# Kernel tuning notes

Hardware: AMD Instinct MI355X
Metric: run time of the kernel (lower is better)

The kernel has to match this reference:

```python
import jax, jax.numpy as jnp
import numpy as np

N_HEADS = 4
ROPE_THETA = 10000.0


def rotate_half(x):
    h = x.shape[-1] // 2
    return jnp.concatenate([-x[..., h:], x[..., :h]], axis=-1)


def setup_inputs() -> dict:
    key = jax.random.key(0)
    k1, k2, k3, k4, k5 = jax.random.split(key, 5)
    B, L, D, M = 4, 2048, 216, 64
    x = jax.random.normal(k1, (B, L, D), dtype=jnp.float32)
    mem_k = jax.random.normal(k2, (B, M, D), dtype=jnp.float32)
    mem_v = jax.random.normal(k3, (B, M, D), dtype=jnp.float32)
    attention_mask = jnp.ones((B, L), dtype=jnp.int32)
    # pre-transposed Linear weights (y = x @ W); scaled for stability
    Wqkv = jax.random.normal(k4, (D, 3 * D), dtype=jnp.float32) * (D ** -0.5)
    Wo = jax.random.normal(k5, (D, D), dtype=jnp.float32) * (D ** -0.5)
    return {"x": x, "mem_k": mem_k, "mem_v": mem_v,
            "attention_mask": attention_mask, "Wqkv": Wqkv, "Wo": Wo}


def reference(x, mem_k, mem_v, attention_mask, Wqkv, Wo):
    B, L, D = x.shape
    H = N_HEADS
    hd = D // H
    scale = hd ** -0.5
    M = mem_k.shape[1]

    # QKV projection -> [B, L, 3, H, hd] -> [B, H, L, hd]
    qkv = (x @ Wqkv).reshape(B, L, 3, H, hd)
    q = jnp.transpose(qkv[:, :, 0], (0, 2, 1, 3))
    k = jnp.transpose(qkv[:, :, 1], (0, 2, 1, 3))
    v = jnp.transpose(qkv[:, :, 2], (0, 2, 1, 3))

    # RoPE (cos/sin: [L, hd], broadcast over B,H)
    inv_freq = 1.0 / (ROPE_THETA ** (jnp.arange(0, hd, 2, dtype=jnp.float32) / hd))
    t = jnp.arange(L, dtype=jnp.float32)
    freqs = jnp.outer(t, inv_freq)
    emb = jnp.concatenate([freqs, freqs], axis=-1)
    cos, sin = jnp.cos(emb), jnp.sin(emb)
    q = q * cos + rotate_half(q) * sin
    k = k * cos + rotate_half(k) * sin

    # memory KV: [B, M, D] -> [B, H, M, hd], prepend along kv axis
    mk = jnp.transpose(mem_k.reshape(B, M, H, hd), (0, 2, 1, 3))
    mv = jnp.transpose(mem_v.reshape(B, M, H, hd), (0, 2, 1, 3))
    k_all = jnp.concatenate([mk, k], axis=2)  # [B, H, M+L, hd]
    v_all = jnp.concatenate([mv, v], axis=2)

    scores = jnp.einsum('bhld,bhmd->bhlm', q, k_all) * scale  # [B,H,L,M+L]

    # causal mask applies only to the self-attention block (cols >= M)
    causal = jnp.triu(jnp.ones((L, L), dtype=bool), k=1)
    full_causal = jnp.concatenate([jnp.zeros((L, M), dtype=bool), causal], axis=1)
    scores = jnp.where(full_causal[None, None], -jnp.inf, scores)

    # padding mask: memory positions always valid
    combined = jnp.concatenate(
        [jnp.ones((B, M), dtype=attention_mask.dtype), attention_mask], axis=-1)
    scores = jnp.where(combined[:, None, None, :] == 0, -jnp.inf, scores)

    attn = jax.nn.softmax(scores, axis=-1)  # dropout is identity in eval
    out = jnp.einsum('bhlm,bhmd->bhld', attn, v_all)
    out = jnp.transpose(out, (0, 2, 1, 3)).reshape(B, L, D)
    return out @ Wo
```

## Files before the change

### kernel.cpp

```cpp
#include <hip/hip_runtime.h>
#include <math.h>

#define B_ 4
#define L_ 2048
#define D_ 216
#define H_ 4
#define HD 54
#define HDP 64
#define M_ 64
#define LK 2112
#define NT_ 33
#define KP 256

typedef __attribute__((ext_vector_type(8))) __bf16 bf16x8;
typedef __attribute__((ext_vector_type(4))) __bf16 bf16x4;
typedef __attribute__((ext_vector_type(4))) float f32x4;

__global__ void conv_x(const float* __restrict__ x, __bf16* __restrict__ xb) {
    int idx = blockIdx.x * 256 + threadIdx.x;
    int row = idx >> 5, c8 = idx & 31;
    bf16x8 v{};
    if (c8 < 27) {
        const float* p = x + (size_t)row * 216 + c8 * 8;
        #pragma unroll
        for (int j = 0; j < 8; ++j) v[j] = (__bf16)p[j];
    }
    *reinterpret_cast<bf16x8*>(xb + (size_t)row * KP + c8 * 8) = v;
}

__global__ void conv_wt(const float* __restrict__ W, __bf16* __restrict__ Wt,
                        int Kin, int Nin, int Npad) {
    int idx = blockIdx.x * 256 + threadIdx.x;
    if (idx >= Npad * KP) return;
    int n = idx >> 8, k = idx & 255;
    float v = (n < Nin && k < Kin) ? W[(size_t)k * Nin + n] : 0.f;
    Wt[idx] = (__bf16)v;
}

__global__ __launch_bounds__(256) void gemm_mfma(const __bf16* __restrict__ A,
                                                 const __bf16* __restrict__ Bt,
                                                 float* __restrict__ C, int N) {
    __shared__ __align__(16) __bf16 As[8192];
    __shared__ __align__(16) __bf16 Bs[4096];
    const int col0 = blockIdx.x * 64;
    const int row0 = blockIdx.y * 128;
    const int tid = threadIdx.x;
    const int lane = tid & 63;
    const int w = tid >> 6, wm = w >> 1, wn = w & 1;
    const int l15 = lane & 15, l4 = lane >> 4;

    f32x4 acc[4][2];
    #pragma unroll
    for (int m = 0; m < 4; ++m)
        #pragma unroll
        for (int n = 0; n < 2; ++n) acc[m][n] = (f32x4){0.f, 0.f, 0.f, 0.f};

    bf16x8 ra[4], rb[2];
    #pragma unroll
    for (int i = 0; i < 4; ++i) { int c = tid + 256 * i, r = c >> 3, c8 = c & 7;
        ra[i] = *reinterpret_cast<const bf16x8*>(A + (size_t)(row0 + r) * KP + c8 * 8); }
    #pragma unroll
    for (int i = 0; i < 2; ++i) { int c = tid + 256 * i, r = c >> 3, c8 = c & 7;
        rb[i] = *reinterpret_cast<const bf16x8*>(Bt + (size_t)(col0 + r) * KP + c8 * 8); }

    for (int kit = 0; kit < 4; ++kit) {
        __syncthreads();
        #pragma unroll
        for (int i = 0; i < 4; ++i) { int c = tid + 256 * i, r = c >> 3, c8 = c & 7;
            *reinterpret_cast<bf16x8*>(&As[r * 64 + ((c8 ^ (r & 7)) * 8)]) = ra[i]; }
        #pragma unroll
        for (int i = 0; i < 2; ++i) { int c = tid + 256 * i, r = c >> 3, c8 = c & 7;
            *reinterpret_cast<bf16x8*>(&Bs[r * 64 + ((c8 ^ (r & 7)) * 8)]) = rb[i]; }
        __syncthreads();
        if (kit < 3) {
            const int k0 = (kit + 1) * 64;
            #pragma unroll
            for (int i = 0; i < 4; ++i) { int c = tid + 256 * i, r = c >> 3, c8 = c & 7;
                ra[i] = *reinterpret_cast<const bf16x8*>(A + (size_t)(row0 + r) * KP + k0 + c8 * 8); }
            #pragma unroll
            for (int i = 0; i < 2; ++i) { int c = tid + 256 * i, r = c >> 3, c8 = c & 7;
                rb[i] = *reinterpret_cast<const bf16x8*>(Bt + (size_t)(col0 + r) * KP + k0 + c8 * 8); }
        }
        #pragma unroll
        for (int ks = 0; ks < 2; ++ks) {
            bf16x8 af[4], bfr[2];
            #pragma unroll
            for (int m = 0; m < 4; ++m) { int row = wm * 64 + m * 16 + l15; int ch = ks * 4 + l4;
                af[m] = *reinterpret_cast<const bf16x8*>(&As[row * 64 + ((ch ^ (row & 7)) * 8)]); }
            #pragma unroll
            for (int n = 0; n < 2; ++n) { int row = wn * 32 + n * 16 + l15; int ch = ks * 4 + l4;
                bfr[n] = *reinterpret_cast<const bf16x8*>(&Bs[row * 64 + ((ch ^ (row & 7)) * 8)]); }
            #pragma unroll
            for (int m = 0; m < 4; ++m)
                #pragma unroll
                for (int n = 0; n < 2; ++n)
                    acc[m][n] = __builtin_amdgcn_mfma_f32_16x16x32_bf16(af[m], bfr[n], acc[m][n], 0, 0, 0);
        }
    }
    #pragma unroll
    for (int m = 0; m < 4; ++m)
        #pragma unroll
        for (int n = 0; n < 2; ++n) {
            int cc = col0 + wn * 32 + n * 16 + l15;
            if (cc < N) {
                #pragma unroll
                for (int rr = 0; rr < 4; ++rr)
                    C[(size_t)(row0 + wm * 64 + m * 16 + l4 * 4 + rr) * N + cc] = acc[m][n][rr];
            }
        }
}

__global__ void memkv_pack(const float* __restrict__ mk, const float* __restrict__ mv,
                           __bf16* __restrict__ kall, __bf16* __restrict__ vt) {
    int idx = blockIdx.x * 256 + threadIdx.x;
    if (idx >= B_ * M_ * H_ * 64) return;
    int b  = idx >> 14;
    int m  = (idx >> 8) & 63;
    int h  = (idx >> 6) & 3;
    int dd = idx & 63;
    float kv = (dd < HD) ? mk[((size_t)(b * M_ + m)) * D_ + h * HD + dd] : 0.f;
    kall[((size_t)(b * 4 + h) * LK + m) * HDP + dd] = (__bf16)kv;
    if (dd < HD)
        vt[((size_t)(b * 4 + h) * HD + dd) * LK + m] =
            (__bf16)mv[((size_t)(b * M_ + m)) * D_ + h * HD + dd];
}

__global__ __launch_bounds__(128) void rope_pack(const float* __restrict__ qkv,
                                                 __bf16* __restrict__ qb,
                                                 __bf16* __restrict__ kall) {
    const int blk = blockIdx.x;
    const int b = blk / L_, l = blk % L_;
    const float* row = qkv + (size_t)blk * 648;
    const int t = threadIdx.x;
    const float scale = 0.19632593f;
    if (t < 108) {
        int h = t / 27, ii = t % 27;
        float inv = exp2f(-0.49213749924f * (float)ii);
        float ang = (float)l * inv;
        float s = sinf(ang), c = cosf(ang);
        float q0v = row[h * HD + ii], q1v = row[h * HD + ii + 27];
        float k0v = row[D_ + h * HD + ii], k1v = row[D_ + h * HD + ii + 27];
        size_t qoff = ((size_t)(b * 4 + h) * L_ + l) * HDP;
        qb[qoff + ii]      = (__bf16)((q0v * c - q1v * s) * scale);
        qb[qoff + ii + 27] = (__bf16)((q1v * c + q0v * s) * scale);
        size_t koff = ((size_t)(b * 4 + h) * LK + M_ + l) * HDP;
        kall[koff + ii]      = (__bf16)(k0v * c - k1v * s);
        kall[koff + ii + 27] = (__bf16)(k1v * c + k0v * s);
    }
    for (int p = t; p < 40; p += 128) {
        int h = p / 10, dd = 54 + p % 10;
        qb[((size_t)(b * 4 + h) * L_ + l) * HDP + dd] = (__bf16)0.f;
        kall[((size_t)(b * 4 + h) * LK + M_ + l) * HDP + dd] = (__bf16)0.f;
    }
}

__global__ __launch_bounds__(256) void transpose_v(const float* __restrict__ qkv,
                                                   __bf16* __restrict__ vt) {
    const int l0 = blockIdx.x * 64;
    const int b = blockIdx.y;
    __shared__ float T[64][55];
    for (int h = 0; h < 4; ++h) {
        __syncthreads();
        for (int idx = threadIdx.x; idx < 64 * 54; idx += 256) {
            int l = idx / 54, d = idx % 54;
            T[l][d] = qkv[((size_t)(b * L_ + l0 + l)) * 648 + 432 + h * 54 + d];
        }
        __syncthreads();
        for (int idx = threadIdx.x; idx < 54 * 64; idx += 256) {
            int d = idx >> 6, l = idx & 63;
            vt[((size_t)(b * 4 + h) * HD + d) * LK + M_ + l0 + l] = (__bf16)T[l][d];
        }
    }
}

__global__ void mask_bias(const int* __restrict__ amask, float* __restrict__ bias) {
    int idx = blockIdx.x * 256 + threadIdx.x;
    if (idx >= B_ * LK) return;
    int b = idx / LK, c = idx % LK;
    bias[idx] = (c < M_ || amask[b * L_ + c - M_] != 0) ? 0.f : -1e30f;
}

__global__ void pad_flags(const int* __restrict__ amask, int* __restrict__ padflag) {
    int t = threadIdx.x;
    if (t >= B_ * NT_) return;
    int b = t / NT_, tile = t % NT_;
    int flag = 0;
    for (int u = 0; u < 64; ++u) {
        int c = tile * 64 + u;
        if (c >= M_ && amask[b * L_ + c - M_] == 0) flag = 1;
    }
    padflag[t] = flag;
}

__global__ __launch_bounds__(256) void flash_mfma(const __bf16* __restrict__ qb,
                                                  const __bf16* __restrict__ kall,
                                                  const __bf16* __restrict__ vt,
                                                  const float* __restrict__ bias,
                                                  const int* __restrict__ padflag,
                                                  __bf16* __restrict__ aoutb) {
    const int qt = (blockIdx.y & 8) ? (31 - (int)blockIdx.x) : (int)blockIdx.x;
    const int q0 = qt * 64;
    const int bh = blockIdx.y;
    const int b = bh >> 2, h = bh & 3;
    __shared__ __align__(16) __bf16 Qs[4096];
    __shared__ __align__(16) __bf16 Ks[4096];
    __shared__ __align__(16) __bf16 Vs[4096];
    __shared__ __align__(16) __bf16 Ps[4096];
    __shared__ float biasS[64];

    const int tid = threadIdx.x;
    const int lane = tid & 63;
    const int w = tid >> 6;
    const int l15 = lane & 15;
    const int l4 = lane >> 4;

    {
        const __bf16* src = qb + ((size_t)bh * L_ + q0) * HDP;
        for (int ch = tid; ch < 512; ch += 256) {
            int row = ch >> 3, c8 = ch & 7;
            bf16x8 v = *reinterpret_cast<const bf16x8*>(src + ch * 8);
            *reinterpret_cast<bf16x8*>(&Qs[row * 64 + ((c8 ^ (row & 7)) * 8)]) = v;
        }
        if (tid < 80) {
            int d = 54 + (tid >> 3), c8 = tid & 7;
            bf16x8 z{};
            *reinterpret_cast<bf16x8*>(&Vs[d * 64 + ((c8 ^ (d & 7)) * 8)]) = z;
        }
    }

    const int ntiles = qt + 2;
    const int rq = q0 + 16 * w + l15;
    const __bf16* kbase = kall + (size_t)bh * LK * HDP;
    const __bf16* vbase = vt + (size_t)bh * HD * LK;

    bf16x8 rk[2], rv[2];
    float biasR = 0.f;
    int flagC;
    {
        rk[0] = *reinterpret_cast<const bf16x8*>(kbase + tid * 8);
        rk[1] = *reinterpret_cast<const bf16x8*>(kbase + (tid + 256) * 8);
        { int d = tid >> 3, c8 = tid & 7;
          rv[0] = *reinterpret_cast<const bf16x8*>(vbase + (size_t)d * LK + c8 * 8); }
        if (tid < 176) { int c = tid + 256, d = c >> 3, c8 = c & 7;
          rv[1] = *reinterpret_cast<const bf16x8*>(vbase + (size_t)d * LK + c8 * 8); }
        if (tid < 64) biasR = bias[b * LK + tid];
        flagC = padflag[b * NT_];
    }

    __syncthreads();
    bf16x8 aQ[2];
    {
        int qrow = 16 * w + l15, s = (qrow & 7) << 3;
        aQ[0] = *reinterpret_cast<const bf16x8*>(&Qs[qrow * 64 + ((l4 * 8) ^ s)]);
        aQ[1] = *reinterpret_cast<const bf16x8*>(&Qs[qrow * 64 + ((32 + l4 * 8) ^ s)]);
    }

    f32x4 Oacc[4];
    #pragma unroll
    for (int nt = 0; nt < 4; ++nt) Oacc[nt] = (f32x4){0.f, 0.f, 0.f, 0.f};
    float m_run = -1e30f, l_run = 0.f;

    for (int t = 0; t < ntiles; ++t) {
        const int cbase = t * 64;
        __syncthreads();
        { int r = tid >> 3, c8 = tid & 7;
          *reinterpret_cast<bf16x8*>(&Ks[r * 64 + ((c8 ^ (r & 7)) * 8)]) = rk[0]; }
        { int c = tid + 256, r = c >> 3, c8 = c & 7;
          *reinterpret_cast<bf16x8*>(&Ks[r * 64 + ((c8 ^ (r & 7)) * 8)]) = rk[1]; }
        { int d = tid >> 3, c8 = tid & 7;
          *reinterpret_cast<bf16x8*>(&Vs[d * 64 + ((c8 ^ (d & 7)) * 8)]) = rv[0]; }
        if (tid < 176) { int c = tid + 256, d = c >> 3, c8 = c & 7;
          *reinterpret_cast<bf16x8*>(&Vs[d * 64 + ((c8 ^ (d & 7)) * 8)]) = rv[1]; }
        if (tid < 64) biasS[tid] = biasR;
        const int flag = flagC;
        __syncthreads();
        if (t + 1 < ntiles) {
            const __bf16* ks = kbase + (size_t)(cbase + 64) * HDP;
            rk[0] = *reinterpret_cast<const bf16x8*>(ks + tid * 8);
            rk[1] = *reinterpret_cast<const bf16x8*>(ks + (tid + 256) * 8);
            { int d = tid >> 3, c8 = tid & 7;
              rv[0] = *reinterpret_cast<const bf16x8*>(vbase + (size_t)d * LK + cbase + 64 + c8 * 8); }
            if (tid < 176) { int c = tid + 256, d = c >> 3, c8 = c & 7;
              rv[1] = *reinterpret_cast<const bf16x8*>(vbase + (size_t)d * LK + cbase + 64 + c8 * 8); }
            if (tid < 64) biasR = bias[b * LK + cbase + 64 + tid];
            flagC = padflag[b * NT_ + t + 1];
        }

        f32x4 S[4];
        #pragma unroll
        for (int nt = 0; nt < 4; ++nt) {
            int krow = nt * 16 + l15, s = (krow & 7) << 3;
            bf16x8 b0 = *reinterpret_cast<const bf16x8*>(&Ks[krow * 64 + ((l4 * 8) ^ s)]);
            bf16x8 b1 = *reinterpret_cast<const bf16x8*>(&Ks[krow * 64 + ((32 + l4 * 8) ^ s)]);
            f32x4 acc = (f32x4){0.f, 0.f, 0.f, 0.f};
            acc = __builtin_amdgcn_mfma_f32_16x16x32_bf16(b0, aQ[0], acc, 0, 0, 0);
            acc = __builtin_amdgcn_mfma_f32_16x16x32_bf16(b1, aQ[1], acc, 0, 0, 0);
            S[nt] = acc;
        }
        if (flag) {
            #pragma unroll
            for (int nt = 0; nt < 4; ++nt)
                #pragma unroll
                for (int r = 0; r < 4; ++r)
                    S[nt][r] += biasS[nt * 16 + l4 * 4 + r];
        }
        if (t == ntiles - 1) {
            #pragma unroll
            for (int nt = 0; nt < 4; ++nt)
                #pragma unroll
                for (int r = 0; r < 4; ++r) {
                    int cg = cbase + nt * 16 + l4 * 4 + r;
                    if (cg > rq + M_) S[nt][r] = -1e30f;
                }
        }
        float mx = fmaxf(fmaxf(S[0][0], S[0][1]), fmaxf(S[0][2], S[0][3]));
        #pragma unroll
        for (int nt = 1; nt < 4; ++nt)
            mx = fmaxf(mx, fmaxf(fmaxf(S[nt][0], S[nt][1]), fmaxf(S[nt][2], S[nt][3])));
        mx = fmaxf(mx, __shfl_xor(mx, 16));
        mx = fmaxf(mx, __shfl_xor(mx, 32));
        float m_new = fmaxf(m_run, mx);
        float alpha = exp2f(m_run - m_new);
        m_run = m_new;
        float ls = 0.f;
        #pragma unroll
        for (int nt = 0; nt < 4; ++nt)
            #pragma unroll
            for (int r = 0; r < 4; ++r) {
                float p = exp2f(S[nt][r] - m_new);
                S[nt][r] = p;
                ls += p;
            }
        ls += __shfl_xor(ls, 16);
        ls += __shfl_xor(ls, 32);
        l_run = l_run * alpha + ls;
        {
            int prow = 16 * w + l15, s = (prow & 7) << 3;
            #pragma unroll
            for (int nt = 0; nt < 4; ++nt) {
                bf16x4 pk;
                pk[0] = (__bf16)S[nt][0]; pk[1] = (__bf16)S[nt][1];
                pk[2] = (__bf16)S[nt][2]; pk[3] = (__bf16)S[nt][3];
                *reinterpret_cast<bf16x4*>(&Ps[prow * 64 + ((nt * 16 + l4 * 4) ^ s)]) = pk;
            }
        }
        float aO[4];
        #pragma unroll
        for (int r = 0; r < 4; ++r)
            aO[r] = __shfl(alpha, (lane & 0x30) | (l4 * 4 + r), 64);
        #pragma unroll
        for (int nt = 0; nt < 4; ++nt)
            #pragma unroll
            for (int r = 0; r < 4; ++r) Oacc[nt][r] *= aO[r];
        bf16x8 aP[2];
        {
            int prow = 16 * w + l15, s = (prow & 7) << 3;
            aP[0] = *reinterpret_cast<const bf16x8*>(&Ps[prow * 64 + ((l4 * 8) ^ s)]);
            aP[1] = *reinterpret_cast<const bf16x8*>(&Ps[prow * 64 + ((32 + l4 * 8) ^ s)]);
        }
        #pragma unroll
        for (int nt = 0; nt < 4; ++nt) {
            int vrow = nt * 16 + l15, s = (vrow & 7) << 3;
            bf16x8 v0 = *reinterpret_cast<const bf16x8*>(&Vs[vrow * 64 + ((l4 * 8) ^ s)]);
            bf16x8 v1 = *reinterpret_cast<const bf16x8*>(&Vs[vrow * 64 + ((32 + l4 * 8) ^ s)]);
            Oacc[nt] = __builtin_amdgcn_mfma_f32_16x16x32_bf16(aP[0], v0, Oacc[nt], 0, 0, 0);
            Oacc[nt] = __builtin_amdgcn_mfma_f32_16x16x32_bf16(aP[1], v1, Oacc[nt], 0, 0, 0);
        }
    }

    float li = 1.f / l_run;
    float invl[4];
    #pragma unroll
    for (int r = 0; r < 4; ++r)
        invl[r] = __shfl(li, (lane & 0x30) | (l4 * 4 + r), 64);
    const int rgbase = q0 + 16 * w + l4 * 4;
    #pragma unroll
    for (int nt = 0; nt < 4; ++nt) {
        int c = nt * 16 + l15;
        if (c < HD) {
            #pragma unroll
            for (int r = 0; r < 4; ++r)
                aoutb[((size_t)b * L_ + rgbase + r) * KP + h * HD + c] =
                    (__bf16)(Oacc[nt][r] * invl[r]);
        }
    }
}

extern "C" void kernel_launch(void* const* d_in, const int* in_sizes, int n_in,
                              void* d_out, int out_size, void* d_ws, size_t ws_size,
                              hipStream_t stream) {
    const float* x     = (const float*)d_in[0];
    const float* mem_k = (const float*)d_in[1];
    const float* mem_v = (const float*)d_in[2];
    const int*   amask = (const int*)d_in[3];
    const float* Wqkv  = (const float*)d_in[4];
    const float* Wo    = (const float*)d_in[5];
    float* out = (float*)d_out;

    char* p = (char*)d_ws;
    float* qkv_raw = (float*)p;        p += (size_t)8192 * 648 * 4;
    float* bias    = (float*)p;        p += (size_t)B_ * LK * 4;
    int*   padflag = (int*)p;          p += (size_t)B_ * NT_ * 4;
    __bf16* xb     = (__bf16*)p;       p += (size_t)8192 * KP * 2;
    __bf16* wqkvt  = (__bf16*)p;       p += (size_t)704 * KP * 2;
    __bf16* wot    = (__bf16*)p;       p += (size_t)256 * KP * 2;
    __bf16* aoutb  = (__bf16*)p;       p += (size_t)8192 * KP * 2;
    __bf16* qb     = (__bf16*)p;       p += (size_t)16 * 2048 * 64 * 2;
    __bf16* kall   = (__bf16*)p;       p += (size_t)16 * 2112 * 64 * 2;
    __bf16* vt     = (__bf16*)p;       p += (size_t)16 * 54 * 2112 * 2;

    conv_x<<<dim3(8192 * 32 / 256), 256, 0, stream>>>(x, xb);
    conv_wt<<<dim3(704), 256, 0, stream>>>(Wqkv, wqkvt, 216, 648, 704);
    conv_wt<<<dim3(256), 256, 0, stream>>>(Wo, wot, 216, 216, 256);

    gemm_mfma<<<dim3(11, 64), 256, 0, stream>>>(xb, wqkvt, qkv_raw, 648);

    memkv_pack<<<dim3((B_ * M_ * H_ * 64 + 255) / 256), 256, 0, stream>>>(mem_k, mem_v, kall, vt);
    rope_pack<<<dim3(B_ * L_), 128, 0, stream>>>(qkv_raw, qb, kall);
    transpose_v<<<dim3(L_ / 64, B_), 256, 0, stream>>>(qkv_raw, vt);
    mask_bias<<<dim3((B_ * LK + 255) / 256), 256, 0, stream>>>(amask, bias);
    pad_flags<<<dim3(1), 256, 0, stream>>>(amask, padflag);

    flash_mfma<<<dim3(32, 16), 256, 0, stream>>>(qb, kall, vt, bias, padflag, aoutb);

    gemm_mfma<<<dim3(4, 64), 256, 0, stream>>>(aoutb, wot, out, 216);
}
```

Measured before the change: 116.0 us.

## Split flash attention over KV chunks, fuse prep kernels, widen GEMM tiles

Merges the conversion, mask and memory-KV packing kernels into a single prep launch, and merges RoPE with the V transpose into one tiled kernel that caches the sin/cos table in shared memory. The GEMM output tile widens from 64 to 128 columns. Flash attention is split along the KV axis into chunks of 8 tiles, so the causal load is spread over 84 blocks per head instead of 32 uneven ones. A new combine kernel merges the partial outputs through their max and sum statistics, at the cost of extra fp32 partial-output traffic and one more launch.

```diff
diff --git a/kernel.cpp b/kernel.cpp
--- a/kernel.cpp
+++ b/kernel.cpp
@@ -11,56 +11,98 @@
 #define LK 2112
 #define NT_ 33
 #define KP 256
+#define SPB 84
 
 typedef __attribute__((ext_vector_type(8))) __bf16 bf16x8;
 typedef __attribute__((ext_vector_type(4))) __bf16 bf16x4;
 typedef __attribute__((ext_vector_type(4))) float f32x4;
 
-__global__ void conv_x(const float* __restrict__ x, __bf16* __restrict__ xb) {
-    int idx = blockIdx.x * 256 + threadIdx.x;
-    int row = idx >> 5, c8 = idx & 31;
-    bf16x8 v{};
-    if (c8 < 27) {
-        const float* p = x + (size_t)row * 216 + c8 * 8;
-        #pragma unroll
-        for (int j = 0; j < 8; ++j) v[j] = (__bf16)p[j];
-    }
-    *reinterpret_cast<bf16x8*>(xb + (size_t)row * KP + c8 * 8) = v;
-}
-
-__global__ void conv_wt(const float* __restrict__ W, __bf16* __restrict__ Wt,
-                        int Kin, int Nin, int Npad) {
-    int idx = blockIdx.x * 256 + threadIdx.x;
-    if (idx >= Npad * KP) return;
-    int n = idx >> 8, k = idx & 255;
-    float v = (n < Nin && k < Kin) ? W[(size_t)k * Nin + n] : 0.f;
-    Wt[idx] = (__bf16)v;
+__global__ __launch_bounds__(256) void prep(const float* __restrict__ x,
+                                            const float* __restrict__ Wqkv,
+                                            const float* __restrict__ Wo,
+                                            const int* __restrict__ amask,
+                                            const float* __restrict__ mk,
+                                            const float* __restrict__ mv,
+                                            __bf16* __restrict__ xb,
+                                            __bf16* __restrict__ wqkvt,
+                                            __bf16* __restrict__ wot,
+                                            float* __restrict__ bias,
+                                            int* __restrict__ padflag,
+                                            __bf16* __restrict__ kall,
+                                            __bf16* __restrict__ vt) {
+    const int bid = blockIdx.x, tid = threadIdx.x;
+    if (bid < 1024) {
+        int idx = bid * 256 + tid;
+        int row = idx >> 5, c8 = idx & 31;
+        bf16x8 v{};
+        if (c8 < 27) {
+            const float* p = x + (size_t)row * 216 + c8 * 8;
+            #pragma unroll
+            for (int j = 0; j < 8; ++j) v[j] = (__bf16)p[j];
+        }
+        *reinterpret_cast<bf16x8*>(xb + (size_t)row * KP + c8 * 8) = v;
+    } else if (bid < 1792) {
+        int idx = (bid - 1024) * 256 + tid;
+        int n = idx >> 8, k = idx & 255;
+        wqkvt[idx] = (__bf16)((n < 648 && k < 216) ? Wqkv[(size_t)k * 648 + n] : 0.f);
+    } else if (bid < 2048) {
+        int idx = (bid - 1792) * 256 + tid;
+        int n = idx >> 8, k = idx & 255;
+        wot[idx] = (__bf16)((n < 216 && k < 216) ? Wo[(size_t)k * 216 + n] : 0.f);
+    } else if (bid < 2081) {
+        int idx = (bid - 2048) * 256 + tid;
+        if (idx < B_ * LK) {
+            int b = idx / LK, c = idx % LK;
+            bias[idx] = (c < M_ || amask[b * L_ + c - M_] != 0) ? 0.f : -1e30f;
+        }
+    } else if (bid == 2081) {
+        if (tid < B_ * NT_) {
+            int b = tid / NT_, tile = tid % NT_;
+            int flag = 0;
+            for (int u = 0; u < 64; ++u) {
+                int c = tile * 64 + u;
+                if (c >= M_ && c < LK && amask[b * L_ + c - M_] == 0) flag = 1;
+            }
+            padflag[tid] = flag;
+        }
+    } else {
+        int idx = (bid - 2082) * 256 + tid;
+        int b  = idx >> 14;
+        int m  = (idx >> 8) & 63;
+        int h  = (idx >> 6) & 3;
+        int dd = idx & 63;
+        float kv = (dd < HD) ? mk[((size_t)(b * M_ + m)) * D_ + h * HD + dd] : 0.f;
+        kall[((size_t)(b * 4 + h) * LK + m) * HDP + dd] = (__bf16)kv;
+        if (dd < HD)
+            vt[((size_t)(b * 4 + h) * HD + dd) * LK + m] =
+                (__bf16)mv[((size_t)(b * M_ + m)) * D_ + h * HD + dd];
+    }
 }
 
 __global__ __launch_bounds__(256) void gemm_mfma(const __bf16* __restrict__ A,
                                                  const __bf16* __restrict__ Bt,
                                                  float* __restrict__ C, int N) {
     __shared__ __align__(16) __bf16 As[8192];
-    __shared__ __align__(16) __bf16 Bs[4096];
-    const int col0 = blockIdx.x * 64;
+    __shared__ __align__(16) __bf16 Bs[8192];
+    const int col0 = blockIdx.x * 128;
     const int row0 = blockIdx.y * 128;
     const int tid = threadIdx.x;
     const int lane = tid & 63;
     const int w = tid >> 6, wm = w >> 1, wn = w & 1;
     const int l15 = lane & 15, l4 = lane >> 4;
 
-    f32x4 acc[4][2];
+    f32x4 acc[4][4];
     #pragma unroll
     for (int m = 0; m < 4; ++m)
         #pragma unroll
-        for (int n = 0; n < 2; ++n) acc[m][n] = (f32x4){0.f, 0.f, 0.f, 0.f};
-
-    bf16x8 ra[4], rb[2];
+        for (int n = 0; n < 4; ++n) acc[m][n] = (f32x4){0.f, 0.f, 0.f, 0.f};
+
+    bf16x8 ra[4], rb[4];
     #pragma unroll
     for (int i = 0; i < 4; ++i) { int c = tid + 256 * i, r = c >> 3, c8 = c & 7;
         ra[i] = *reinterpret_cast<const bf16x8*>(A + (size_t)(row0 + r) * KP + c8 * 8); }
     #pragma unroll
-    for (int i = 0; i < 2; ++i) { int c = tid + 256 * i, r = c >> 3, c8 = c & 7;
+    for (int i = 0; i < 4; ++i) { int c = tid + 256 * i, r = c >> 3, c8 = c & 7;
         rb[i] = *reinterpret_cast<const bf16x8*>(Bt + (size_t)(col0 + r) * KP + c8 * 8); }
 
     for (int kit = 0; kit < 4; ++kit) {
@@ -69,7 +111,7 @@
         for (int i = 0; i < 4; ++i) { int c = tid + 256 * i, r = c >> 3, c8 = c & 7;
             *reinterpret_cast<bf16x8*>(&As[r * 64 + ((c8 ^ (r & 7)) * 8)]) = ra[i]; }
         #pragma unroll
-        for (int i = 0; i < 2; ++i) { int c = tid + 256 * i, r = c >> 3, c8 = c & 7;
+        for (int i = 0; i < 4; ++i) { int c = tid + 256 * i, r = c >> 3, c8 = c & 7;
             *reinterpret_cast<bf16x8*>(&Bs[r * 64 + ((c8 ^ (r & 7)) * 8)]) = rb[i]; }
         __syncthreads();
         if (kit < 3) {
@@ -78,30 +120,30 @@
             for (int i = 0; i < 4; ++i) { int c = tid + 256 * i, r = c >> 3, c8 = c & 7;
                 ra[i] = *reinterpret_cast<const bf16x8*>(A + (size_t)(row0 + r) * KP + k0 + c8 * 8); }
             #pragma unroll
-            for (int i = 0; i < 2; ++i) { int c = tid + 256 * i, r = c >> 3, c8 = c & 7;
+            for (int i = 0; i < 4; ++i) { int c = tid + 256 * i, r = c >> 3, c8 = c & 7;
                 rb[i] = *reinterpret_cast<const bf16x8*>(Bt + (size_t)(col0 + r) * KP + k0 + c8 * 8); }
         }
         #pragma unroll
         for (int ks = 0; ks < 2; ++ks) {
-            bf16x8 af[4], bfr[2];
+            bf16x8 af[4], bfr[4];
             #pragma unroll
             for (int m = 0; m < 4; ++m) { int row = wm * 64 + m * 16 + l15; int ch = ks * 4 + l4;
                 af[m] = *reinterpret_cast<const bf16x8*>(&As[row * 64 + ((ch ^ (row & 7)) * 8)]); }
             #pragma unroll
-            for (int n = 0; n < 2; ++n) { int row = wn * 32 + n * 16 + l15; int ch = ks * 4 + l4;
+            for (int n = 0; n < 4; ++n) { int row = wn * 64 + n * 16 + l15; int ch = ks * 4 + l4;
                 bfr[n] = *reinterpret_cast<const bf16x8*>(&Bs[row * 64 + ((ch ^ (row & 7)) * 8)]); }
             #pragma unroll
             for (int m = 0; m < 4; ++m)
                 #pragma unroll
-                for (int n = 0; n < 2; ++n)
+                for (int n = 0; n < 4; ++n)
                     acc[m][n] = __builtin_amdgcn_mfma_f32_16x16x32_bf16(af[m], bfr[n], acc[m][n], 0, 0, 0);
         }
     }
     #pragma unroll
     for (int m = 0; m < 4; ++m)
         #pragma unroll
-        for (int n = 0; n < 2; ++n) {
-            int cc = col0 + wn * 32 + n * 16 + l15;
+        for (int n = 0; n < 4; ++n) {
+            int cc = col0 + wn * 64 + n * 16 + l15;
             if (cc < N) {
                 #pragma unroll
                 for (int rr = 0; rr < 4; ++rr)
@@ -110,98 +152,78 @@
         }
 }
 
-__global__ void memkv_pack(const float* __restrict__ mk, const float* __restrict__ mv,
-                           __bf16* __restrict__ kall, __bf16* __restrict__ vt) {
-    int idx = blockIdx.x * 256 + threadIdx.x;
-    if (idx >= B_ * M_ * H_ * 64) return;
-    int b  = idx >> 14;
-    int m  = (idx >> 8) & 63;
-    int h  = (idx >> 6) & 3;
-    int dd = idx & 63;
-    float kv = (dd < HD) ? mk[((size_t)(b * M_ + m)) * D_ + h * HD + dd] : 0.f;
-    kall[((size_t)(b * 4 + h) * LK + m) * HDP + dd] = (__bf16)kv;
-    if (dd < HD)
-        vt[((size_t)(b * 4 + h) * HD + dd) * LK + m] =
-            (__bf16)mv[((size_t)(b * M_ + m)) * D_ + h * HD + dd];
-}
-
-__global__ __launch_bounds__(128) void rope_pack(const float* __restrict__ qkv,
-                                                 __bf16* __restrict__ qb,
-                                                 __bf16* __restrict__ kall) {
-    const int blk = blockIdx.x;
-    const int b = blk / L_, l = blk % L_;
-    const float* row = qkv + (size_t)blk * 648;
-    const int t = threadIdx.x;
+__global__ __launch_bounds__(256) void rope_tv(const float* __restrict__ qkv,
+                                               __bf16* __restrict__ qb,
+                                               __bf16* __restrict__ kall,
+                                               __bf16* __restrict__ vt) {
+    const int l0 = blockIdx.x * 64, b = blockIdx.y;
+    __shared__ float SN[64][27], CN[64][27];
+    __shared__ float T[64][55];
+    const int tid = threadIdx.x;
+    for (int idx = tid; idx < 64 * 27; idx += 256) {
+        int row = idx / 27, ii = idx % 27;
+        float inv = exp2f(-0.49213749924f * (float)ii);
+        float ang = (float)(l0 + row) * inv;
+        SN[row][ii] = sinf(ang);
+        CN[row][ii] = cosf(ang);
+    }
+    __syncthreads();
     const float scale = 0.19632593f;
-    if (t < 108) {
-        int h = t / 27, ii = t % 27;
-        float inv = exp2f(-0.49213749924f * (float)ii);
-        float ang = (float)l * inv;
-        float s = sinf(ang), c = cosf(ang);
-        float q0v = row[h * HD + ii], q1v = row[h * HD + ii + 27];
-        float k0v = row[D_ + h * HD + ii], k1v = row[D_ + h * HD + ii + 27];
-        size_t qoff = ((size_t)(b * 4 + h) * L_ + l) * HDP;
+    for (int idx = tid; idx < 64 * 108; idx += 256) {
+        int row = idx / 108, p = idx % 108, h = p / 27, ii = p % 27;
+        const float* rp = qkv + (size_t)(b * L_ + l0 + row) * 648;
+        float s = SN[row][ii], c = CN[row][ii];
+        float q0v = rp[h * HD + ii], q1v = rp[h * HD + ii + 27];
+        float k0v = rp[D_ + h * HD + ii], k1v = rp[D_ + h * HD + ii + 27];
+        size_t qoff = ((size_t)(b * 4 + h) * L_ + l0 + row) * HDP;
         qb[qoff + ii]      = (__bf16)((q0v * c - q1v * s) * scale);
         qb[qoff + ii + 27] = (__bf16)((q1v * c + q0v * s) * scale);
-        size_t koff = ((size_t)(b * 4 + h) * LK + M_ + l) * HDP;
+        size_t koff = ((size_t)(b * 4 + h) * LK + M_ + l0 + row) * HDP;
         kall[koff + ii]      = (__bf16)(k0v * c - k1v * s);
         kall[koff + ii + 27] = (__bf16)(k1v * c + k0v * s);
     }
-    for (int p = t; p < 40; p += 128) {
-        int h = p / 10, dd = 54 + p % 10;
-        qb[((size_t)(b * 4 + h) * L_ + l) * HDP + dd] = (__bf16)0.f;
-        kall[((size_t)(b * 4 + h) * LK + M_ + l) * HDP + dd] = (__bf16)0.f;
-    }
-}
-
-__global__ __launch_bounds__(256) void transpose_v(const float* __restrict__ qkv,
-                                                   __bf16* __restrict__ vt) {
-    const int l0 = blockIdx.x * 64;
-    const int b = blockIdx.y;
-    __shared__ float T[64][55];
+    for (int idx = tid; idx < 64 * 40; idx += 256) {
+        int row = idx / 40, p = idx % 40, h = p / 10, dd = 54 + p % 10;
+        qb[((size_t)(b * 4 + h) * L_ + l0 + row) * HDP + dd] = (__bf16)0.f;
+        kall[((size_t)(b * 4 + h) * LK + M_ + l0 + row) * HDP + dd] = (__bf16)0.f;
+    }
     for (int h = 0; h < 4; ++h) {
         __syncthreads();
-        for (int idx = threadIdx.x; idx < 64 * 54; idx += 256) {
+        for (int idx = tid; idx < 64 * 54; idx += 256) {
             int l = idx / 54, d = idx % 54;
             T[l][d] = qkv[((size_t)(b * L_ + l0 + l)) * 648 + 432 + h * 54 + d];
         }
         __syncthreads();
-        for (int idx = threadIdx.x; idx < 54 * 64; idx += 256) {
+        for (int idx = tid; idx < 54 * 64; idx += 256) {
             int d = idx >> 6, l = idx & 63;
             vt[((size_t)(b * 4 + h) * HD + d) * LK + M_ + l0 + l] = (__bf16)T[l][d];
         }
     }
 }
 
-__global__ void mask_bias(const int* __restrict__ amask, float* __restrict__ bias) {
-    int idx = blockIdx.x * 256 + threadIdx.x;
-    if (idx >= B_ * LK) return;
-    int b = idx / LK, c = idx % LK;
-    bias[idx] = (c < M_ || amask[b * L_ + c - M_] != 0) ? 0.f : -1e30f;
-}
-
-__global__ void pad_flags(const int* __restrict__ amask, int* __restrict__ padflag) {
-    int t = threadIdx.x;
-    if (t >= B_ * NT_) return;
-    int b = t / NT_, tile = t % NT_;
-    int flag = 0;
-    for (int u = 0; u < 64; ++u) {
-        int c = tile * 64 + u;
-        if (c >= M_ && amask[b * L_ + c - M_] == 0) flag = 1;
-    }
-    padflag[t] = flag;
-}
-
-__global__ __launch_bounds__(256) void flash_mfma(const __bf16* __restrict__ qb,
-                                                  const __bf16* __restrict__ kall,
-                                                  const __bf16* __restrict__ vt,
-                                                  const float* __restrict__ bias,
-                                                  const int* __restrict__ padflag,
-                                                  __bf16* __restrict__ aoutb) {
-    const int qt = (blockIdx.y & 8) ? (31 - (int)blockIdx.x) : (int)blockIdx.x;
+__global__ __launch_bounds__(256) void flash_split(const __bf16* __restrict__ qb,
+                                                   const __bf16* __restrict__ kall,
+                                                   const __bf16* __restrict__ vt,
+                                                   const float* __restrict__ bias,
+                                                   const int* __restrict__ padflag,
+                                                   float* __restrict__ op,
+                                                   float* __restrict__ ml) {
+    int qt = 31, sp = 0;
+    {
+        int sidx = blockIdx.x, accq = 0;
+        for (int q = 0; q < 32; ++q) {
+            int c = (q + 9) >> 3;
+            if (sidx < accq + c) { qt = q; sp = sidx - accq; break; }
+            accq += c;
+        }
+    }
+    const int pb = blockIdx.y * SPB + blockIdx.x;
     const int q0 = qt * 64;
     const int bh = blockIdx.y;
-    const int b = bh >> 2, h = bh & 3;
+    const int b = bh >> 2;
+    const int tstart = sp * 8;
+    const int tend = min(tstart + 8, qt + 2);
+
     __shared__ __align__(16) __bf16 Qs[4096];
     __shared__ __align__(16) __bf16 Ks[4096];
     __shared__ __align__(16) __bf16 Vs[4096];
@@ -228,7 +250,6 @@
         }
     }
 
-    const int ntiles = qt + 2;
     const int rq = q0 + 16 * w + l15;
     const __bf16* kbase = kall + (size_t)bh * LK * HDP;
     const __bf16* vbase = vt + (size_t)bh * HD * LK;
@@ -237,14 +258,15 @@
     float biasR = 0.f;
     int flagC;
     {
-        rk[0] = *reinterpret_cast<const bf16x8*>(kbase + tid * 8);
-        rk[1] = *reinterpret_cast<const bf16x8*>(kbase + (tid + 256) * 8);
+        const __bf16* ks = kbase + (size_t)tstart * 64 * HDP;
+        rk[0] = *reinterpret_cast<const bf16x8*>(ks + tid * 8);
+        rk[1] = *reinterpret_cast<const bf16x8*>(ks + (tid + 256) * 8);
         { int d = tid >> 3, c8 = tid & 7;
-          rv[0] = *reinterpret_cast<const bf16x8*>(vbase + (size_t)d * LK + c8 * 8); }
+          rv[0] = *reinterpret_cast<const bf16x8*>(vbase + (size_t)d * LK + tstart * 64 + c8 * 8); }
         if (tid < 176) { int c = tid + 256, d = c >> 3, c8 = c & 7;
-          rv[1] = *reinterpret_cast<const bf16x8*>(vbase + (size_t)d * LK + c8 * 8); }
-        if (tid < 64) biasR = bias[b * LK + tid];
-        flagC = padflag[b * NT_];
+          rv[1] = *reinterpret_cast<const bf16x8*>(vbase + (size_t)d * LK + tstart * 64 + c8 * 8); }
+        if (tid < 64) biasR = bias[b * LK + tstart * 64 + tid];
+        flagC = padflag[b * NT_ + tstart];
     }
 
     __syncthreads();
@@ -260,7 +282,7 @@
     for (int nt = 0; nt < 4; ++nt) Oacc[nt] = (f32x4){0.f, 0.f, 0.f, 0.f};
     float m_run = -1e30f, l_run = 0.f;
 
-    for (int t = 0; t < ntiles; ++t) {
+    for (int t = tstart; t < tend; ++t) {
         const int cbase = t * 64;
         __syncthreads();
         { int r = tid >> 3, c8 = tid & 7;
@@ -274,7 +296,7 @@
         if (tid < 64) biasS[tid] = biasR;
         const int flag = flagC;
         __syncthreads();
-        if (t + 1 < ntiles) {
+        if (t + 1 < tend) {
             const __bf16* ks = kbase + (size_t)(cbase + 64) * HDP;
             rk[0] = *reinterpret_cast<const bf16x8*>(ks + tid * 8);
             rk[1] = *reinterpret_cast<const bf16x8*>(ks + (tid + 256) * 8);
@@ -304,7 +326,7 @@
                 for (int r = 0; r < 4; ++r)
                     S[nt][r] += biasS[nt * 16 + l4 * 4 + r];
         }
-        if (t == ntiles - 1) {
+        if (t == qt + 1) {
             #pragma unroll
             for (int nt = 0; nt < 4; ++nt)
                 #pragma unroll
@@ -368,21 +390,50 @@
         }
     }
 
-    float li = 1.f / l_run;
-    float invl[4];
-    #pragma unroll
-    for (int r = 0; r < 4; ++r)
-        invl[r] = __shfl(li, (lane & 0x30) | (l4 * 4 + r), 64);
-    const int rgbase = q0 + 16 * w + l4 * 4;
+    if (l4 == 0) {
+        ml[((size_t)pb * 64 + 16 * w + l15) * 2 + 0] = m_run;
+        ml[((size_t)pb * 64 + 16 * w + l15) * 2 + 1] = l_run;
+    }
     #pragma unroll
     for (int nt = 0; nt < 4; ++nt) {
         int c = nt * 16 + l15;
         if (c < HD) {
             #pragma unroll
             for (int r = 0; r < 4; ++r)
-                aoutb[((size_t)b * L_ + rgbase + r) * KP + h * HD + c] =
-                    (__bf16)(Oacc[nt][r] * invl[r]);
-        }
+                op[((size_t)pb * HD + c) * 64 + 16 * w + l4 * 4 + r] = Oacc[nt][r];
+        }
+    }
+}
+
+__global__ __launch_bounds__(64) void combine(const float* __restrict__ op,
+                                              const float* __restrict__ ml,
+                                              __bf16* __restrict__ aoutb) {
+    const int qt = blockIdx.x, bh = blockIdx.y;
+    const int b = bh >> 2, h = bh & 3;
+    const int ns = (qt + 9) >> 3;
+    int accq = 0;
+    for (int q = 0; q < qt; ++q) accq += (q + 9) >> 3;
+    const int pb0 = bh * SPB + accq;
+    const int row = threadIdx.x;
+
+    float mi[5], li[5];
+    float m = -1e30f;
+    for (int i = 0; i < ns; ++i) {
+        mi[i] = ml[((size_t)(pb0 + i) * 64 + row) * 2 + 0];
+        li[i] = ml[((size_t)(pb0 + i) * 64 + row) * 2 + 1];
+        m = fmaxf(m, mi[i]);
+    }
+    float wgt[5], Lr = 0.f;
+    for (int i = 0; i < ns; ++i) {
+        wgt[i] = exp2f(mi[i] - m);
+        Lr += li[i] * wgt[i];
+    }
+    float inv = 1.f / Lr;
+    for (int d = 0; d < HD; ++d) {
+        float o = 0.f;
+        for (int i = 0; i < ns; ++i)
+            o += wgt[i] * op[((size_t)(pb0 + i) * HD + d) * 64 + row];
+        aoutb[((size_t)(b * L_) + qt * 64 + row) * KP + h * HD + d] = (__bf16)(o * inv);
     }
 }
 
@@ -402,26 +453,21 @@
     float* bias    = (float*)p;        p += (size_t)B_ * LK * 4;
     int*   padflag = (int*)p;          p += (size_t)B_ * NT_ * 4;
     __bf16* xb     = (__bf16*)p;       p += (size_t)8192 * KP * 2;
-    __bf16* wqkvt  = (__bf16*)p;       p += (size_t)704 * KP * 2;
+    __bf16* wqkvt  = (__bf16*)p;       p += (size_t)768 * KP * 2;
     __bf16* wot    = (__bf16*)p;       p += (size_t)256 * KP * 2;
     __bf16* aoutb  = (__bf16*)p;       p += (size_t)8192 * KP * 2;
     __bf16* qb     = (__bf16*)p;       p += (size_t)16 * 2048 * 64 * 2;
     __bf16* kall   = (__bf16*)p;       p += (size_t)16 * 2112 * 64 * 2;
     __bf16* vt     = (__bf16*)p;       p += (size_t)16 * 54 * 2112 * 2;
-
-    conv_x<<<dim3(8192 * 32 / 256), 256, 0, stream>>>(x, xb);
-    conv_wt<<<dim3(704), 256, 0, stream>>>(Wqkv, wqkvt, 216, 648, 704);
-    conv_wt<<<dim3(256), 256, 0, stream>>>(Wo, wot, 216, 216, 256);
-
-    gemm_mfma<<<dim3(11, 64), 256, 0, stream>>>(xb, wqkvt, qkv_raw, 648);
-
-    memkv_pack<<<dim3((B_ * M_ * H_ * 64 + 255) / 256), 256, 0, stream>>>(mem_k, mem_v, kall, vt);
-    rope_pack<<<dim3(B_ * L_), 128, 0, stream>>>(qkv_raw, qb, kall);
-    transpose_v<<<dim3(L_ / 64, B_), 256, 0, stream>>>(qkv_raw, vt);
-    mask_bias<<<dim3((B_ * LK + 255) / 256), 256, 0, stream>>>(amask, bias);
-    pad_flags<<<dim3(1), 256, 0, stream>>>(amask, padflag);
-
-    flash_mfma<<<dim3(32, 16), 256, 0, stream>>>(qb, kall, vt, bias, padflag, aoutb);
-
-    gemm_mfma<<<dim3(4, 64), 256, 0, stream>>>(aoutb, wot, out, 216);
-}
+    float* opbuf = qkv_raw;
+    float* mlbuf = qkv_raw + (size_t)16 * SPB * HD * 64;
+
+    prep<<<dim3(2338), 256, 0, stream>>>(x, Wqkv, Wo, amask, mem_k, mem_v,
+                                         xb, wqkvt, wot, bias, padflag, kall, vt);
+    gemm_mfma<<<dim3(6, 64), 256, 0, stream>>>(xb, wqkvt, qkv_raw, 648);
+    rope_tv<<<dim3(32, 4), 256, 0, stream>>>(qkv_raw, qb, kall, vt);
+    flash_split<<<dim3(SPB, 16), 256, 0, stream>>>(qb, kall, vt, bias, padflag,
+                                                   opbuf, mlbuf);
+    combine<<<dim3(32, 16), 64, 0, stream>>>(opbuf, mlbuf, aoutb);
+    gemm_mfma<<<dim3(2, 64), 256, 0, stream>>>(aoutb, wot, out, 216);
+}
```

New measurement: 182.8 us. 57.6% more time.
